# Kernel tuning notes

Hardware: AMD Instinct MI355X
Metric: run time of the kernel (lower is better)

The kernel has to match this reference:

```python
import jax, jax.numpy as jnp
import numpy as np

VOCAB = 32000
EMBED = 256
HIDDEN = 512
BATCH = 64
SEQ = 512


def setup_inputs() -> dict:
    key = jax.random.key(0)
    k1, k2, k3, k4, k5, k6 = jax.random.split(key, 6)
    s = 1.0 / np.sqrt(HIDDEN)
    return {
        "source": jax.random.randint(k1, (BATCH, SEQ), 0, VOCAB),
        "embedding": jax.random.normal(k2, (VOCAB, EMBED), dtype=jnp.float32),
        "W_ih": jax.random.uniform(k3, (EMBED, HIDDEN), dtype=jnp.float32, minval=-s, maxval=s),
        "W_hh": jax.random.uniform(k4, (HIDDEN, HIDDEN), dtype=jnp.float32, minval=-s, maxval=s),
        "b_ih": jax.random.uniform(k5, (HIDDEN,), dtype=jnp.float32, minval=-s, maxval=s),
        "b_hh": jax.random.uniform(k6, (HIDDEN,), dtype=jnp.float32, minval=-s, maxval=s),
    }


def reference(source, embedding, W_ih, W_hh, b_ih, b_hh):
    # Embedding lookup: (B, S, E)
    embedded = embedding[source]
    batch_size = source.shape[0]
    h0 = jnp.zeros((batch_size, HIDDEN), dtype=embedding.dtype)

    def step(h, x_t):
        # Elman RNN cell: h' = tanh(x W_ih + b_ih + h W_hh + b_hh)
        h_new = jnp.tanh(x_t @ W_ih + b_ih + h @ W_hh + b_hh)
        return h_new, h_new

    # scan over time axis: xs shape (S, B, E)
    _, hiddens = jax.lax.scan(step, h0, jnp.swapaxes(embedded, 0, 1))
    # hiddens: (S, B, H) -> (B, S, H)
    return jnp.swapaxes(hiddens, 0, 1)
```

## Files before the change

kernel.cpp:

```cpp
#include <hip/hip_runtime.h>
#include <stdint.h>

#define EMBED  256
#define HIDDEN 512
#define BATCH  64
#define SEQ    512

typedef _Float16 f16x8 __attribute__((ext_vector_type(8)));
typedef _Float16 f16x4 __attribute__((ext_vector_type(4)));
typedef float    f32x4 __attribute__((ext_vector_type(4)));


#define WIH_FRAGS (8 * 32 * 64 * 8)
#define WHH_FRAGS (16 * 32 * 64 * 8)

__global__ void prep_pack(const float* __restrict__ W_ih,
                          const float* __restrict__ W_hh,
                          unsigned short* __restrict__ wih_p,
                          unsigned short* __restrict__ whh_p) {
    int tid = blockIdx.x * blockDim.x + threadIdx.x;
    if (tid < WIH_FRAGS) {
        int j = tid & 7, l = (tid >> 3) & 63, nt = (tid >> 9) & 31, s = tid >> 14;
        int k   = s * 32 + ((l >> 4) << 3) + j;
        int col = (nt << 4) + (l & 15);
        wih_p[tid] = __builtin_bit_cast(unsigned short, (_Float16)W_ih[k * HIDDEN + col]);
    } else {
        int t2 = tid - WIH_FRAGS;
        if (t2 < WHH_FRAGS) {
            int j = t2 & 7, l = (t2 >> 3) & 63, mt = (t2 >> 9) & 31, s = t2 >> 14;
            int k   = s * 32 + ((l >> 4) << 3) + j;
            int col = (mt << 4) + (l & 15);
            whh_p[t2] = __builtin_bit_cast(unsigned short, (_Float16)W_hh[k * HIDDEN + col]);
        }
    }
}

__global__ __launch_bounds__(256) void enc_gemm_ih(
    const int* __restrict__ source,
    const float* __restrict__ embedding,
    const unsigned short* __restrict__ wih_p,
    const float* __restrict__ b_ih,
    const float* __restrict__ b_hh,
    float* __restrict__ out)
{
    const int lane = threadIdx.x & 63;
    const int mt   = (blockIdx.x << 2) + (threadIdx.x >> 6);
    const int r0   = mt << 4;
    const int g    = lane >> 4;
    const int c    = lane & 15;

    const int idx = source[r0 + c];
    const float* erow = embedding + (size_t)idx * EMBED;

    f16x8 afrag[8];
#pragma unroll
    for (int s = 0; s < 8; ++s) {
        const float* p = erow + (s << 5) + (g << 3);
        f32x4 f0 = *(const f32x4*)p;
        f32x4 f1 = *(const f32x4*)(p + 4);
        f16x8 a;
        a[0] = (_Float16)f0[0]; a[1] = (_Float16)f0[1];
        a[2] = (_Float16)f0[2]; a[3] = (_Float16)f0[3];
        a[4] = (_Float16)f1[0]; a[5] = (_Float16)f1[1];
        a[6] = (_Float16)f1[2]; a[7] = (_Float16)f1[3];
        afrag[s] = a;
    }

    const f16x8* wp = (const f16x8*)wih_p;
    for (int nt = 0; nt < 32; ++nt) {
        f32x4 acc = {0.f, 0.f, 0.f, 0.f};
#pragma unroll
        for (int s = 0; s < 8; ++s) {
            f16x8 bfr = wp[(((s << 5) + nt) << 6) + lane];
            acc = __builtin_amdgcn_mfma_f32_16x16x32_f16(afrag[s], bfr, acc, 0, 0, 0);
        }
        const int col  = (nt << 4) + c;
        const float bias = b_ih[col] + b_hh[col];
        char* ob = (char*)out + (size_t)(r0 + (g << 2)) * 2048 + 1024 + (col << 1);
#pragma unroll
        for (int r = 0; r < 4; ++r)
            *(_Float16*)(ob + (size_t)r * 2048) = (_Float16)(acc[r] + bias);
    }
}

__global__ __launch_bounds__(512, 1) void enc_rnn(
    const unsigned short* __restrict__ whh_p,
    float* __restrict__ out)
{
    extern __shared__ char lds[];
    char* hbase = lds;
    char* wbase = lds + 16384;

    const int tid  = threadIdx.x;
    const int lane = tid & 63;
    const int w    = tid >> 6;
    const int g    = lane >> 4;
    const int c    = lane & 15;
    const int cc   = lane & 7;
    const bool cvalid = (c < 8);
    const int mtg0 = w << 2;

    const f16x8* wp = (const f16x8*)whh_p;

    {
        char* wl = wbase + ((w * 18) << 10) + (lane << 4);
#pragma unroll
        for (int fid = 0; fid < 18; ++fid) {
            int s = (fid < 2) ? 8 : 9 + ((fid - 2) >> 2);
            int m = (fid < 2) ? 2 + fid : ((fid - 2) & 3);
            f16x8 v = wp[((s * 32 + mtg0 + m) << 6) + lane];
            *(f16x8*)(wl + (fid << 10)) = v;
        }
    }
    for (int i = tid; i < 16384 / 4; i += 512) ((int*)hbase)[i] = 0;

    f16x8 wreg[34];
#pragma unroll
    for (int s = 0; s < 8; ++s)
#pragma unroll
        for (int m = 0; m < 4; ++m)
            wreg[s * 4 + m] = wp[((s * 32 + mtg0 + m) << 6) + lane];
#pragma unroll
    for (int m = 0; m < 2; ++m)
        wreg[32 + m] = wp[((8 * 32 + mtg0 + m) << 6) + lane];

    __syncthreads();

    char* hev = hbase + (cc << 10) + ((cc >> 2) << 6) + ((g ^ (cc & 3)) << 4);
    char* hod = hbase + (cc << 10) + (((cc >> 2) ^ 1) << 6) + ((g ^ (cc & 3)) << 4);
    char* hw[4];
#pragma unroll
    for (int m = 0; m < 4; ++m) {
        int u = (w << 3) + (m << 1) + (g >> 1);
        hw[m] = hbase + (cc << 10) + ((u ^ cc) << 4) + ((g & 1) << 3);
    }
    char* ga = (char*)out + (size_t)((blockIdx.x << 3) + cc) * SEQ * 2048
             + (w << 7) + (g << 3);
    const char* sp0 = (const char*)whh_p + ((13 * 32 + mtg0) << 10) + (lane << 4);
    const char* sp1 = (const char*)whh_p + ((14 * 32 + mtg0) << 10) + (lane << 4);
    const char* sp2 = (const char*)whh_p + ((15 * 32 + mtg0) << 10) + (lane << 4);
    char* wl = wbase + ((w * 18) << 10) + (lane << 4);

    auto STEP = [&](int RB, int RBN, int TB) {
        f16x8 sA[4], sB[4], sC[4];
#pragma unroll
        for (int m = 0; m < 4; ++m) sA[m] = *(const f16x8*)(sp0 + (m << 10));
#pragma unroll
        for (int m = 0; m < 4; ++m) sB[m] = *(const f16x8*)(sp1 + (m << 10));
        f16x4 pre[4];
#pragma unroll
        for (int m = 0; m < 4; ++m)
            pre[m] = *(const f16x4*)(ga + TB + 1024 + (m << 5));

        f32x4 acc[4];
#pragma unroll
        for (int m = 0; m < 4; ++m) acc[m] = (f32x4){0.f, 0.f, 0.f, 0.f};

        f16x8 hh[16];
        hh[0] = *(const f16x8*)(hev + RB);
        hh[1] = *(const f16x8*)(hod + (0 << 7) + RB);
#pragma unroll
        for (int s = 0; s < 16; ++s) {
            if (s + 2 < 16) {
                int sn = s + 2;
                hh[sn] = *(const f16x8*)(((sn & 1) ? hod : hev) + ((sn >> 1) << 7) + RB);
            }
            if (s == 9) {
#pragma unroll
                for (int m = 0; m < 4; ++m) sC[m] = *(const f16x8*)(sp2 + (m << 10));
            }
#pragma unroll
            for (int m = 0; m < 4; ++m) {
                f16x8 wv;
                if (s < 8)            wv = wreg[s * 4 + m];
                else if (s == 8 && m < 2) wv = wreg[32 + m];
                else if (s == 8)      wv = *(const f16x8*)(wl + ((m - 2) << 10));
                else if (s < 13)      wv = *(const f16x8*)(wl + ((2 + ((s - 9) << 2) + m) << 10));
                else if (s == 13)     wv = sA[m];
                else if (s == 14)     wv = sB[m];
                else                  wv = sC[m];
                acc[m] = __builtin_amdgcn_mfma_f32_16x16x32_f16(wv, hh[s], acc[m], 0, 0, 0);
            }
        }

#pragma unroll
        for (int m = 0; m < 4; ++m) {
            f16x4 hv;
#pragma unroll
            for (int r = 0; r < 4; ++r) {
                float x  = acc[m][r] + (float)pre[m][r];
                float e  = __expf(2.0f * x);
                float th = 1.0f - 2.0f * __builtin_amdgcn_rcpf(e + 1.0f);
                hv[r] = (_Float16)th;
            }
            if (cvalid) {
                *(f16x4*)(ga + TB + (m << 5)) = hv;
                *(f16x4*)(hw[m] + RBN) = hv;
            }
        }
        __syncthreads();
    };

#pragma unroll 1
    for (int tp = 0; tp < SEQ; tp += 2) {
        STEP(0, 8192, 0);
        STEP(8192, 0, 2048);
        ga += 4096;
    }
}

__global__ __launch_bounds__(256) void expand_rows(float* __restrict__ out) {
    const int lane = threadIdx.x & 63;
    const int row  = (blockIdx.x << 2) + (threadIdx.x >> 6);
    char* rp = (char*)out + ((size_t)row << 11);
    f16x8 v = *(const f16x8*)(rp + (lane << 4));
    f32x4 lo, hi;
#pragma unroll
    for (int i = 0; i < 4; ++i) { lo[i] = (float)v[i]; hi[i] = (float)v[i + 4]; }
    *(f32x4*)(rp + (lane << 5))      = lo;
    *(f32x4*)(rp + (lane << 5) + 16) = hi;
}

extern "C" void kernel_launch(void* const* d_in, const int* in_sizes, int n_in,
                              void* d_out, int out_size, void* d_ws, size_t ws_size,
                              hipStream_t stream) {
    const int*   source    = (const int*)d_in[0];
    const float* embedding = (const float*)d_in[1];
    const float* W_ih      = (const float*)d_in[2];
    const float* W_hh      = (const float*)d_in[3];
    const float* b_ih      = (const float*)d_in[4];
    const float* b_hh      = (const float*)d_in[5];
    float* out = (float*)d_out;

    unsigned short* wih_p = (unsigned short*)d_ws;
    unsigned short* whh_p = wih_p + WIH_FRAGS;

    prep_pack<<<(WIH_FRAGS + WHH_FRAGS) / 256, 256, 0, stream>>>(W_ih, W_hh, wih_p, whh_p);
    enc_gemm_ih<<<512, 256, 0, stream>>>(source, embedding, wih_p, b_ih, b_hh, out);
    enc_rnn<<<8, 512, 163840, stream>>>(whh_p, out);
    expand_rows<<<8192, 256, 0, stream>>>(out);
}
```

Baseline: 1.082 ms.

## Process 16 batch rows per RNN block on four blocks using full MFMA width

The recurrent kernel now runs 16 batch rows per workgroup, filling all 16 columns of each MFMA tile instead of 8. It therefore launches 4 workgroups instead of 8. The hidden-state LDS buffer doubles and the swizzles are reworked. W_hh placement is rebalanced: 36 fragments stay in registers (pinned with empty asm), 12 go to LDS, and 4 are streamed from global memory. This halves the wasted MFMA work per step, but each block now does twice the per-step work and only 4 CUs are used, so the serial recurrence latency per step may grow.

```diff
diff --git a/kernel.cpp b/kernel.cpp
--- a/kernel.cpp
+++ b/kernel.cpp
@@ -89,64 +89,64 @@
 {
     extern __shared__ char lds[];
     char* hbase = lds;
-    char* wbase = lds + 16384;
+    char* wbase = lds + 32768;
 
     const int tid  = threadIdx.x;
     const int lane = tid & 63;
     const int w    = tid >> 6;
     const int g    = lane >> 4;
     const int c    = lane & 15;
-    const int cc   = lane & 7;
-    const bool cvalid = (c < 8);
-    const int mtg0 = w << 2;
+    const int cx   = c & 7;
+    const int mt0  = w << 2;
 
     const f16x8* wp = (const f16x8*)whh_p;
 
     {
-        char* wl = wbase + ((w * 18) << 10) + (lane << 4);
-#pragma unroll
-        for (int fid = 0; fid < 18; ++fid) {
-            int s = (fid < 2) ? 8 : 9 + ((fid - 2) >> 2);
-            int m = (fid < 2) ? 2 + fid : ((fid - 2) & 3);
-            f16x8 v = wp[((s * 32 + mtg0 + m) << 6) + lane];
-            *(f16x8*)(wl + (fid << 10)) = v;
-        }
-    }
-    for (int i = tid; i < 16384 / 4; i += 512) ((int*)hbase)[i] = 0;
-
-    f16x8 wreg[34];
-#pragma unroll
-    for (int s = 0; s < 8; ++s)
+        char* wl0 = wbase + ((w * 12) << 10) + (lane << 4);
+#pragma unroll
+        for (int fid = 0; fid < 12; ++fid) {
+            int s = 9 + (fid >> 2), m = fid & 3;
+            *(f16x8*)(wl0 + (fid << 10)) = wp[((s * 32 + mt0 + m) << 6) + lane];
+        }
+    }
+    for (int i = tid; i < 32768 / 4; i += 512) ((int*)hbase)[i] = 0;
+
+    f16x8 wreg[36];
+#pragma unroll
+    for (int s = 0; s < 9; ++s)
 #pragma unroll
         for (int m = 0; m < 4; ++m)
-            wreg[s * 4 + m] = wp[((s * 32 + mtg0 + m) << 6) + lane];
-#pragma unroll
-    for (int m = 0; m < 2; ++m)
-        wreg[32 + m] = wp[((8 * 32 + mtg0 + m) << 6) + lane];
+            wreg[s * 4 + m] = wp[((s * 32 + mt0 + m) << 6) + lane];
+#pragma unroll
+    for (int i = 0; i < 36; ++i)
+        asm volatile("" : "+v"(wreg[i]));
 
     __syncthreads();
 
-    char* hev = hbase + (cc << 10) + ((cc >> 2) << 6) + ((g ^ (cc & 3)) << 4);
-    char* hod = hbase + (cc << 10) + (((cc >> 2) ^ 1) << 6) + ((g ^ (cc & 3)) << 4);
+    const int ch = cx >> 2;
+    char* hb2 = hbase + (c << 10) + ((g ^ (cx & 3)) << 4);
+    char* hev = hb2 + (ch << 6);
+    char* hod = hb2 - (ch << 6);
     char* hw[4];
 #pragma unroll
     for (int m = 0; m < 4; ++m) {
-        int u = (w << 3) + (m << 1) + (g >> 1);
-        hw[m] = hbase + (cc << 10) + ((u ^ cc) << 4) + ((g & 1) << 3);
-    }
-    char* ga = (char*)out + (size_t)((blockIdx.x << 3) + cc) * SEQ * 2048
+        int u = (w << 3) | ((m ^ (cx >> 1)) << 1) | ((g >> 1) ^ (cx & 1));
+        hw[m] = hbase + (c << 10) + (u << 4) + ((g & 1) << 3);
+    }
+    char* ga = (char*)out + (size_t)((blockIdx.x << 4) + c) * SEQ * 2048
              + (w << 7) + (g << 3);
-    const char* sp0 = (const char*)whh_p + ((13 * 32 + mtg0) << 10) + (lane << 4);
-    const char* sp1 = (const char*)whh_p + ((14 * 32 + mtg0) << 10) + (lane << 4);
-    const char* sp2 = (const char*)whh_p + ((15 * 32 + mtg0) << 10) + (lane << 4);
-    char* wl = wbase + ((w * 18) << 10) + (lane << 4);
+    const char* sp12 = (const char*)whh_p + ((12 * 32 + mt0) << 10) + (lane << 4);
+    const char* sp13 = (const char*)whh_p + ((13 * 32 + mt0) << 10) + (lane << 4);
+    const char* sp14 = (const char*)whh_p + ((14 * 32 + mt0) << 10) + (lane << 4);
+    const char* sp15 = (const char*)whh_p + ((15 * 32 + mt0) << 10) + (lane << 4);
+    char* wl = wbase + ((w * 12) << 10) + (lane << 4);
 
     auto STEP = [&](int RB, int RBN, int TB) {
         f16x8 sA[4], sB[4], sC[4];
 #pragma unroll
-        for (int m = 0; m < 4; ++m) sA[m] = *(const f16x8*)(sp0 + (m << 10));
-#pragma unroll
-        for (int m = 0; m < 4; ++m) sB[m] = *(const f16x8*)(sp1 + (m << 10));
+        for (int m = 0; m < 4; ++m) sA[m] = *(const f16x8*)(sp12 + (m << 10));
+#pragma unroll
+        for (int m = 0; m < 4; ++m) sB[m] = *(const f16x8*)(sp13 + (m << 10));
         f16x4 pre[4];
 #pragma unroll
         for (int m = 0; m < 4; ++m)
@@ -156,30 +156,27 @@
 #pragma unroll
         for (int m = 0; m < 4; ++m) acc[m] = (f32x4){0.f, 0.f, 0.f, 0.f};
 
-        f16x8 hh[16];
-        hh[0] = *(const f16x8*)(hev + RB);
-        hh[1] = *(const f16x8*)(hod + (0 << 7) + RB);
 #pragma unroll
         for (int s = 0; s < 16; ++s) {
-            if (s + 2 < 16) {
-                int sn = s + 2;
-                hh[sn] = *(const f16x8*)(((sn & 1) ? hod : hev) + ((sn >> 1) << 7) + RB);
-            }
-            if (s == 9) {
-#pragma unroll
-                for (int m = 0; m < 4; ++m) sC[m] = *(const f16x8*)(sp2 + (m << 10));
+            f16x8 h = *(const f16x8*)(((s & 1) ? hod : hev) + (s << 6) + RB);
+            if (s == 6) {
+#pragma unroll
+                for (int m = 0; m < 4; ++m) sC[m] = *(const f16x8*)(sp14 + (m << 10));
             }
 #pragma unroll
             for (int m = 0; m < 4; ++m) {
                 f16x8 wv;
-                if (s < 8)            wv = wreg[s * 4 + m];
-                else if (s == 8 && m < 2) wv = wreg[32 + m];
-                else if (s == 8)      wv = *(const f16x8*)(wl + ((m - 2) << 10));
-                else if (s < 13)      wv = *(const f16x8*)(wl + ((2 + ((s - 9) << 2) + m) << 10));
-                else if (s == 13)     wv = sA[m];
-                else if (s == 14)     wv = sB[m];
-                else                  wv = sC[m];
-                acc[m] = __builtin_amdgcn_mfma_f32_16x16x32_f16(wv, hh[s], acc[m], 0, 0, 0);
+                if (s < 9)        wv = wreg[s * 4 + m];
+                else if (s < 12)  wv = *(const f16x8*)(wl + ((((s - 9) << 2) | m) << 10));
+                else if (s == 12) wv = sA[m];
+                else if (s == 13) wv = sB[m];
+                else if (s == 14) wv = sC[m];
+                else              wv = sA[m];
+                acc[m] = __builtin_amdgcn_mfma_f32_16x16x32_f16(wv, h, acc[m], 0, 0, 0);
+            }
+            if (s == 12) {
+#pragma unroll
+                for (int m = 0; m < 4; ++m) sA[m] = *(const f16x8*)(sp15 + (m << 10));
             }
         }
 
@@ -190,21 +187,18 @@
             for (int r = 0; r < 4; ++r) {
                 float x  = acc[m][r] + (float)pre[m][r];
                 float e  = __expf(2.0f * x);
-                float th = 1.0f - 2.0f * __builtin_amdgcn_rcpf(e + 1.0f);
-                hv[r] = (_Float16)th;
-            }
-            if (cvalid) {
-                *(f16x4*)(ga + TB + (m << 5)) = hv;
-                *(f16x4*)(hw[m] + RBN) = hv;
-            }
+                hv[r] = (_Float16)(1.0f - 2.0f * __builtin_amdgcn_rcpf(e + 1.0f));
+            }
+            *(f16x4*)(ga + TB + (m << 5)) = hv;
+            *(f16x4*)(hw[m] + RBN) = hv;
         }
         __syncthreads();
     };
 
 #pragma unroll 1
     for (int tp = 0; tp < SEQ; tp += 2) {
-        STEP(0, 8192, 0);
-        STEP(8192, 0, 2048);
+        STEP(0, 16384, 0);
+        STEP(16384, 0, 2048);
         ga += 4096;
     }
 }
@@ -237,6 +231,6 @@
 
     prep_pack<<<(WIH_FRAGS + WHH_FRAGS) / 256, 256, 0, stream>>>(W_ih, W_hh, wih_p, whh_p);
     enc_gemm_ih<<<512, 256, 0, stream>>>(source, embedding, wih_p, b_ih, b_hh, out);
-    enc_rnn<<<8, 512, 163840, stream>>>(whh_p, out);
+    enc_rnn<<<4, 512, 131072, stream>>>(whh_p, out);
     expand_rows<<<8192, 256, 0, stream>>>(out);
 }
```

After: 1.299 ms. 20.0% more time.
